# Kernel tuning notes

Measured on AMD Instinct MI355X. Metric: run time of the kernel, lower is better.

## Reference

```python
import jax, jax.numpy as jnp
import numpy as np

T, B, C, N, H = 10, 128, 512, 16, 16
D = C // H          # head dim = 32
HID = 2048          # mlp hidden = 4*dim
TAU, THR, SCALE, ALPHA_MIX = 2.0, 1.0, 0.25, 0.5
SG_ALPHA = 4.0      # surrogate sigmoid alpha

@jax.custom_vjp
def spike_fn(x):
    # heaviside forward, sigmoid surrogate backward (MyGrad / sigmoid.apply)
    return (x > 0).astype(x.dtype)

def _spike_fwd(x):
    return spike_fn(x), x

def _spike_bwd(x, g):
    s = jax.nn.sigmoid(SG_ALPHA * x)
    return (g * SG_ALPHA * s * (1.0 - s),)

spike_fn.defvjp(_spike_fwd, _spike_bwd)

def lif(x):
    # multi-step LIF over leading T axis; mem_detach=True => no BPTT through mem
    def step(mem, inp):
        mem = jax.lax.stop_gradient(mem)
        mem = mem + (inp - mem) / TAU
        s = spike_fn(mem - THR)
        mem = mem * (1.0 - jax.lax.stop_gradient(s))
        return mem, s
    return jax.lax.scan(step, jnp.zeros_like(x[0]), x)[1]

def lif_step(mem, inp):
    # single-step LIF (step=1, layer_by_layer=False); state persists across calls
    mem = jax.lax.stop_gradient(mem)
    mem = mem + (inp - mem) / TAU
    s = spike_fn(mem - THR)
    mem = mem * (1.0 - jax.lax.stop_gradient(s))
    return s, mem

def bn(x, p):
    # eval-mode BatchNorm1d over channel dim; x: (T,B,C,N), p: (4,C)=gamma,beta,mean,var
    g, b, m, v = p
    inv = g * jax.lax.rsqrt(v + 1e-5)
    return (x - m[None, None, :, None]) * inv[None, None, :, None] + b[None, None, :, None]

def conv1x1(x, W):
    # Conv1d k=1 == channel GEMM; x: (T,B,Cin,N), W: (Cout,Cin)
    return jnp.einsum('oc,tbcn->tbon', W, x)

def ssa(x, Wq, bn_q, Wk, bn_k, Wv, bn_v, Wproj, bn_proj, ti_w, ti_b):
    def qkv(W, p):
        y = lif(bn(conv1x1(x, W), p))                       # (T,B,C,N) spikes
        # faithful to torch: raw reshape (T,B,C,N)->(T,B,N,H,D) then permute
        return y.reshape(T, B, N, H, D).transpose(0, 1, 3, 2, 4)  # (T,B,H,N,D)
    q = qkv(Wq, bn_q)
    k = qkv(Wk, bn_k)
    v = qkv(Wv, bn_v)

    out0 = (q[0] @ jnp.swapaxes(k[0], -2, -1) * SCALE) @ v[0]   # (B,H,N,D)

    def step(carry, qkv_t):
        q_ti, mem1, mem2 = carry
        qt, kt, vt = qkv_t
        c = q_ti.reshape(B * H, N, D)
        c = jax.lax.conv_general_dilated(
            c, ti_w, (1,), ((2, 2),), dimension_numbers=('NCH', 'OIH', 'NCH'))
        c = c + ti_b[None, :, None]
        c = c.reshape(B, H, N, D)
        s1, mem1 = lif_step(mem1, c)
        mix = s1 * ALPHA_MIX + qt * (1.0 - ALPHA_MIX)
        s2, mem2 = lif_step(mem2, mix)
        attn = (s2 @ jnp.swapaxes(kt, -2, -1) * SCALE) @ vt
        return (s2, mem1, mem2), attn

    init = (q[0], jnp.zeros_like(q[0]), jnp.zeros_like(q[0]))
    _, outs = jax.lax.scan(step, init, (q[1:], k[1:], v[1:]))
    out = jnp.concatenate([out0[None], outs], axis=0)           # (T,B,H,N,D)

    y = jnp.swapaxes(out, 3, 4).reshape(T, B, C, N)
    y = lif(y)                                                  # attn_lif
    y = lif(bn(conv1x1(y, Wproj), bn_proj))                     # proj
    return y

def mlp(x, W1, b1, bn1, W2, b2, bn2):
    h = lif(bn(conv1x1(x, W1) + b1[None, None, :, None], bn1))
    return lif(bn(conv1x1(h, W2) + b2[None, None, :, None], bn2))

def block(x, Wq, Wk, Wv, Wproj, bn_q, bn_k, bn_v, bn_proj, ti_w, ti_b,
          W1, b1, bn1, W2, b2, bn2):
    x = x + ssa(x, Wq, bn_q, Wk, bn_k, Wv, bn_v, Wproj, bn_proj, ti_w, ti_b)
    x = x + mlp(x, W1, b1, bn1, W2, b2, bn2)
    return x

def setup_inputs() -> dict:
    key = jax.random.key(0)
    ks = jax.random.split(key, 16)

    def w(k, o, i):
        return (jax.random.normal(k, (o, i), jnp.float32) / np.float32(np.sqrt(i)))

    def bnp(k, c):
        k1, k2, k3, k4 = jax.random.split(k, 4)
        return jnp.stack([
            jax.random.uniform(k1, (c,), jnp.float32) + 0.5,   # gamma
            jax.random.normal(k2, (c,), jnp.float32) * 0.1,    # beta
            jax.random.normal(k3, (c,), jnp.float32) * 0.1,    # running mean
            jax.random.uniform(k4, (c,), jnp.float32) + 0.5,   # running var
        ])

    return {
        'x': jax.random.normal(ks[0], (T, B, C, N), jnp.float32),
        'Wq': w(ks[1], C, C), 'Wk': w(ks[2], C, C), 'Wv': w(ks[3], C, C),
        'Wproj': w(ks[4], C, C),
        'bn_q': bnp(ks[5], C), 'bn_k': bnp(ks[6], C), 'bn_v': bnp(ks[7], C),
        'bn_proj': bnp(ks[8], C),
        'ti_w': jax.random.normal(ks[9], (16, 16, 5), jnp.float32) / np.float32(np.sqrt(16 * 5)),
        'ti_b': jax.random.normal(ks[10], (16,), jnp.float32) * 0.1,
        'W1': w(ks[11], HID, C), 'b1': jax.random.normal(ks[12], (HID,), jnp.float32) * 0.1,
        'bn1': bnp(ks[13], HID),
        'W2': w(ks[14], C, HID), 'b2': jax.random.normal(ks[15], (C,), jnp.float32) * 0.1,
        'bn2': bnp(jax.random.fold_in(key, 99), C),
    }

def reference(x, Wq, Wk, Wv, Wproj, bn_q, bn_k, bn_v, bn_proj, ti_w, ti_b,
              W1, b1, bn1, W2, b2, bn2):
    return block(x, Wq, Wk, Wv, Wproj, bn_q, bn_k, bn_v, bn_proj, ti_w, ti_b,
                 W1, b1, bn1, W2, b2, bn2)
```

## Files before the change

kernel.cpp:

```cpp
#include <hip/hip_runtime.h>
#include <cstdint>
#include <cstddef>

#define T_   10
#define B_   128
#define CH_  512
#define N_   16
#define H_   16
#define HID_ 2048
#define TB_  (T_ * B_)

#define EP_QKV  0
#define EP_SPK  1
#define EP_HS   2
#define EP_OUT  3

typedef __attribute__((ext_vector_type(8))) short bf16x8;
typedef __attribute__((ext_vector_type(4))) float f32x4;
typedef unsigned short u16;
typedef unsigned long long u64;

__device__ __forceinline__ short f2b(float f) {
    uint32_t u = __float_as_uint(f);
    return (short)((u + 0x7FFFu + ((u >> 16) & 1u)) >> 16);
}
__device__ __forceinline__ float b2f(short s) {
    return __uint_as_float(((uint32_t)(uint16_t)s) << 16);
}

__global__ void fold2(const float* __restrict__ W, const float* __restrict__ bnp,
                      const float* __restrict__ eb, int M, int K, int o0,
                      short* __restrict__ Ah, short* __restrict__ Al,
                      float* __restrict__ bias) {
    int idx = blockIdx.x * 256 + threadIdx.x;
    if (idx >= M * K) return;
    int o = idx / K, k = idx - o * K;
    float g  = bnp[o];
    float be = bnp[M + o];
    float mu = bnp[2 * M + o];
    float va = bnp[3 * M + o];
    float inv = g * (1.0f / sqrtf(va + 1e-5f));
    float w = W[idx] * inv;
    short h = f2b(w);
    Ah[(size_t)(o0 + o) * K + k] = h;
    Al[(size_t)(o0 + o) * K + k] = f2b(w - b2f(h));
    if (k == 0) bias[o0 + o] = ((eb ? eb[o] : 0.0f) - mu) * inv + be;
}

__global__ __launch_bounds__(256) void splitx(
    const float* __restrict__ X, const u16* __restrict__ S,
    short* __restrict__ Bh, short* __restrict__ Bl) {
    __shared__ float xs[8192];
    const int slab = blockIdx.x;
    const int tid  = threadIdx.x;
    const int t    = slab / B_;
    const int b    = slab - t * B_;
    const float* xp = X + (size_t)slab * 8192;
    for (int i = tid; i < 2048; i += 256) {
        float4 v = *(const float4*)&xp[i * 4];
        if (S) {
            union { u16 s[4]; uint2 v; } sw;
            sw.v = *(const uint2*)&S[(size_t)b * 8192 + i * 4];
            v.x += (float)((sw.s[0] >> t) & 1);
            v.y += (float)((sw.s[1] >> t) & 1);
            v.z += (float)((sw.s[2] >> t) & 1);
            v.w += (float)((sw.s[3] >> t) & 1);
        }
        *(float4*)&xs[i * 4] = v;
    }
    __syncthreads();
    const int n = tid & 15, kc = tid >> 4;
    size_t orow = ((size_t)slab * 16 + n) * 512 + kc * 32;
#pragma unroll
    for (int i8 = 0; i8 < 4; ++i8) {
        union { short s[8]; uint4 v; } hb, lb;
#pragma unroll
        for (int j = 0; j < 8; ++j) {
            float v = xs[(kc * 32 + i8 * 8 + j) * 16 + n];
            short h = f2b(v);
            hb.s[j] = h;
            lb.s[j] = f2b(v - b2f(h));
        }
        *(uint4*)&Bh[orow + i8 * 8] = hb.v;
        *(uint4*)&Bl[orow + i8 * 8] = lb.v;
    }
}

template <int R, int GX, int EPI>
__global__ __launch_bounds__(256, 2) void gemm_bf16t(
    const short* __restrict__ Ah, const short* __restrict__ Al,
    const float* __restrict__ bias,
    const short* __restrict__ Bh, const short* __restrict__ Bl,
    u16* __restrict__ O0, u16* __restrict__ O1, u16* __restrict__ O2) {
    constexpr int KT = 512;
    __shared__ __align__(16) short BsH[6400];
    __shared__ __align__(16) short BsL[6400];
    const int tid  = threadIdx.x;
    const int lane = tid & 63;
    const int wv   = tid >> 6;
    const int fid  = blockIdx.x;
    const int xcd  = fid & 7;
    const int slot = fid >> 3;
    const int brow = slot / GX;
    const int xb   = slot - brow * GX;
    const int b    = (brow << 3) | xcd;
    const int l15  = lane & 15;
    const int q    = lane >> 4;
    const int row0 = xb * (R * 64) + wv * (R * 16);

    const int i0 = tid, i1 = tid + 256, i2 = tid + 512;
    auto gaddr = [&](int idx, int k0) -> size_t {
        int qu = idx & 3, n = (idx >> 2) & 15, t = idx >> 6;
        return ((size_t)(t * B_ + b) * 16 + n) * KT + k0 + qu * 8;
    };
    auto laddr = [&](int idx) -> int {
        int qu = idx & 3, n = (idx >> 2) & 15, t = idx >> 6;
        return (t * 16 + n) * 40 + qu * 8;
    };

    f32x4 acc[R][10];
#pragma unroll
    for (int r = 0; r < R; ++r)
#pragma unroll
        for (int t = 0; t < 10; ++t) acc[r][t] = 0.0f;

    uint4 ph0, ph1, ph2, pl0, pl1, pl2;
    ph0 = *(const uint4*)&Bh[gaddr(i0, 0)];
    pl0 = *(const uint4*)&Bl[gaddr(i0, 0)];
    ph1 = *(const uint4*)&Bh[gaddr(i1, 0)];
    pl1 = *(const uint4*)&Bl[gaddr(i1, 0)];
    if (tid < 128) {
        ph2 = *(const uint4*)&Bh[gaddr(i2, 0)];
        pl2 = *(const uint4*)&Bl[gaddr(i2, 0)];
    }

    for (int k0 = 0; k0 < KT; k0 += 32) {
        __syncthreads();
        *(uint4*)&BsH[laddr(i0)] = ph0;
        *(uint4*)&BsL[laddr(i0)] = pl0;
        *(uint4*)&BsH[laddr(i1)] = ph1;
        *(uint4*)&BsL[laddr(i1)] = pl1;
        if (tid < 128) {
            *(uint4*)&BsH[laddr(i2)] = ph2;
            *(uint4*)&BsL[laddr(i2)] = pl2;
        }
        __syncthreads();
        if (k0 + 32 < KT) {
            ph0 = *(const uint4*)&Bh[gaddr(i0, k0 + 32)];
            pl0 = *(const uint4*)&Bl[gaddr(i0, k0 + 32)];
            ph1 = *(const uint4*)&Bh[gaddr(i1, k0 + 32)];
            pl1 = *(const uint4*)&Bl[gaddr(i1, k0 + 32)];
            if (tid < 128) {
                ph2 = *(const uint4*)&Bh[gaddr(i2, k0 + 32)];
                pl2 = *(const uint4*)&Bl[gaddr(i2, k0 + 32)];
            }
        }
        bf16x8 ah[R], al[R];
#pragma unroll
        for (int r = 0; r < R; ++r) {
            size_t ga = (size_t)(row0 + r * 16 + l15) * KT + k0 + q * 8;
            ah[r] = *(const bf16x8*)&Ah[ga];
            al[r] = *(const bf16x8*)&Al[ga];
        }
#pragma unroll
        for (int t = 0; t < 10; ++t) {
            bf16x8 bh = *(const bf16x8*)&BsH[(t * 16 + l15) * 40 + q * 8];
            bf16x8 bl = *(const bf16x8*)&BsL[(t * 16 + l15) * 40 + q * 8];
#pragma unroll
            for (int r = 0; r < R; ++r) {
                acc[r][t] = __builtin_amdgcn_mfma_f32_16x16x32_bf16(ah[r], bh, acc[r][t], 0, 0, 0);
                acc[r][t] = __builtin_amdgcn_mfma_f32_16x16x32_bf16(al[r], bh, acc[r][t], 0, 0, 0);
                acc[r][t] = __builtin_amdgcn_mfma_f32_16x16x32_bf16(ah[r], bl, acc[r][t], 0, 0, 0);
            }
        }
    }

    const int tok = l15;
#pragma unroll
    for (int r = 0; r < R; ++r) {
        u16 m4[4];
#pragma unroll
        for (int reg = 0; reg < 4; ++reg) {
            const int row = row0 + r * 16 + q * 4 + reg;
            const float bsv = bias[row];
            float mem = 0.0f;
            u16 msk = 0;
#pragma unroll
            for (int t = 0; t < 10; ++t) {
                float u = acc[r][t][reg] + bsv;
                mem += (u - mem) * 0.5f;
                bool s = mem > 1.0f;
                if (s) mem = 0.0f;
                msk |= (u16)((s ? 1u : 0u) << t);
            }
            if constexpr (EPI == EP_QKV) {
                int tsr = row >> 9;
                int c   = row & 511;
                int hh  = (c & 31) >> 1;
                int dd  = ((c & 1) << 4) | tok;
                int nn  = c >> 5;
                u16* qp = (tsr == 0) ? O0 : ((tsr == 1) ? O1 : O2);
                qp[(size_t)b * 8192 + (size_t)hh * 512 + dd * 16 + nn] = msk;
            } else {
                m4[reg] = msk;
            }
        }
        if constexpr (EPI == EP_HS) {
            union { u16 s[4]; uint2 v; } pk;
            pk.s[0] = m4[0]; pk.s[1] = m4[1]; pk.s[2] = m4[2]; pk.s[3] = m4[3];
            *(uint2*)&O0[((size_t)b * 16 + tok) * 2048 + row0 + r * 16 + q * 4] = pk.v;
        }
    }
}

template <int R, int GX, int EPI, int KT>
__global__ __launch_bounds__(256, 2) void gemm_pkt(
    const short* __restrict__ Ah, const short* __restrict__ Al,
    const float* __restrict__ bias, const u16* __restrict__ Bu,
    u16* __restrict__ O0, float* __restrict__ Oout,
    const float* __restrict__ Xr, const u16* __restrict__ Sr) {
    constexpr int K8 = KT / 8;
    __shared__ __align__(16) u16 Bp[K8 * 136];
    const int tid  = threadIdx.x;
    const int lane = tid & 63;
    const int wv   = tid >> 6;
    const int fid  = blockIdx.x;
    const int xcd  = fid & 7;
    const int slot = fid >> 3;
    const int brow = slot / GX;
    const int xb   = slot - brow * GX;
    const int b    = (brow << 3) | xcd;
    const int l15  = lane & 15;
    const int q    = lane >> 4;
    const int row0 = xb * (R * 64) + wv * (R * 16);

    for (int idx = tid; idx < 16 * K8; idx += 256) {
        int kc = idx & (K8 - 1), n = idx / K8;
        *(uint4*)&Bp[kc * 136 + n * 8] =
            *(const uint4*)&Bu[((size_t)b * 16 + n) * KT + kc * 8];
    }
    __syncthreads();

    f32x4 acc[R][10];
#pragma unroll
    for (int r = 0; r < R; ++r)
#pragma unroll
        for (int t = 0; t < 10; ++t) acc[r][t] = 0.0f;

    for (int k0 = 0; k0 < KT; k0 += 32) {
        bf16x8 ah[R], al[R];
#pragma unroll
        for (int r = 0; r < R; ++r) {
            size_t ga = (size_t)(row0 + r * 16 + l15) * KT + k0 + q * 8;
            ah[r] = *(const bf16x8*)&Ah[ga];
            al[r] = *(const bf16x8*)&Al[ga];
        }
        union { uint32_t u[4]; uint4 v; } w;
        w.v = *(const uint4*)&Bp[(k0 / 8 + q) * 136 + l15 * 8];
#pragma unroll
        for (int t = 0; t < 10; ++t) {
            union { uint32_t u[4]; bf16x8 h; } bh;
#pragma unroll
            for (int j = 0; j < 4; ++j)
                bh.u[j] = ((w.u[j] >> t) & 0x00010001u) * 0x3F80u;
#pragma unroll
            for (int r = 0; r < R; ++r) {
                acc[r][t] = __builtin_amdgcn_mfma_f32_16x16x32_bf16(ah[r], bh.h, acc[r][t], 0, 0, 0);
                acc[r][t] = __builtin_amdgcn_mfma_f32_16x16x32_bf16(al[r], bh.h, acc[r][t], 0, 0, 0);
            }
        }
    }

    const int tok = l15;
#pragma unroll
    for (int r = 0; r < R; ++r) {
#pragma unroll
        for (int reg = 0; reg < 4; ++reg) {
            const int row = row0 + r * 16 + q * 4 + reg;
            const float bsv = bias[row];
            u16 sv = 0;
            if constexpr (EPI == EP_OUT) sv = Sr[(size_t)b * 8192 + (size_t)row * 16 + tok];
            float mem = 0.0f;
            u16 msk = 0;
#pragma unroll
            for (int t = 0; t < 10; ++t) {
                float u = acc[r][t][reg] + bsv;
                mem += (u - mem) * 0.5f;
                bool s = mem > 1.0f;
                if (s) mem = 0.0f;
                msk |= (u16)((s ? 1u : 0u) << t);
                if constexpr (EPI == EP_OUT) {
                    size_t off = (size_t)(t * B_ + b) * 8192 + (size_t)row * 16 + tok;
                    Oout[off] = Xr[off] + (float)((sv >> t) & 1) + (s ? 1.0f : 0.0f);
                }
            }
            if constexpr (EPI == EP_SPK) {
                O0[(size_t)b * 8192 + (size_t)row * 16 + tok] = msk;
            }
        }
    }
}

__global__ __launch_bounds__(256, 1) void scan_kernel(
    const u16* __restrict__ qs, const u16* __restrict__ ks,
    const u16* __restrict__ vs, const float* __restrict__ tiw,
    const float* __restrict__ tib, u16* __restrict__ y1pk) {
    __shared__ float qS[4][36 * 20];
    __shared__ float kS[4][32 * 20];
    __shared__ float vS[4][32 * 20];
    __shared__ float qbS[4][32 * 20];
    __shared__ float A[4][16 * 17];
    const int l  = threadIdx.x & 63;
    const int w  = threadIdx.x >> 6;
    const int b  = blockIdx.y;
    const int h  = blockIdx.x * 4 + w;
    const int n  = l & 15, dg = l >> 4;
    float* qSw  = qS[w];
    float* kSw  = kS[w];
    float* vSw  = vS[w];
    float* qbSw = qbS[w];
    float* Aw   = A[w];

    float wreg[80];
#pragma unroll
    for (int j = 0; j < 80; ++j) wreg[j] = tiw[n * 80 + j];
    const float tibr = tib[n];

    if (l < 40) { qSw[l] = 0.0f; qSw[680 + l] = 0.0f; }

    const size_t base = (size_t)b * 8192 + (size_t)h * 512 + (size_t)l * 8;
    union { u16 s[8]; uint4 v; } qw, kw, vw;
    qw.v = *(const uint4*)&qs[base];
    kw.v = *(const uint4*)&ks[base];
    vw.v = *(const uint4*)&vs[base];

#pragma unroll
    for (int j = 0; j < 8; ++j) {
        int f = l * 8 + j, d = f >> 4, m = f & 15;
        qSw[(d + 2) * 20 + m] = (float)(qw.s[j] & 1);
        kSw[d * 20 + m]       = (float)(kw.s[j] & 1);
        vSw[d * 20 + m]       = (float)(vw.s[j] & 1);
    }

    float mem1[8] = {}, mem2[8] = {}, mem3[8] = {};
    u16 ym[8] = {};

    auto attn_step = [&](int t) {
        float dots[4] = {0.0f, 0.0f, 0.0f, 0.0f};
#pragma unroll
        for (int d = 0; d < 32; ++d) {
            float qv = qSw[(d + 2) * 20 + n];
#pragma unroll
            for (int jj = 0; jj < 4; ++jj)
                dots[jj] = fmaf(qv, kSw[d * 20 + dg * 4 + jj], dots[jj]);
        }
#pragma unroll
        for (int jj = 0; jj < 4; ++jj) Aw[n * 17 + dg * 4 + jj] = dots[jj] * 0.25f;
        float o[8] = {};
#pragma unroll
        for (int m = 0; m < 16; ++m) {
            float av = Aw[n * 17 + m];
#pragma unroll
            for (int dd = 0; dd < 8; ++dd)
                o[dd] = fmaf(av, vSw[(dg * 8 + dd) * 20 + m], o[dd]);
        }
#pragma unroll
        for (int dd = 0; dd < 8; ++dd) {
            mem3[dd] += (o[dd] - mem3[dd]) * 0.5f;
            bool s3 = mem3[dd] > 1.0f;
            if (s3) mem3[dd] = 0.0f;
            ym[dd] |= (u16)((s3 ? 1u : 0u) << t);
        }
    };

    attn_step(0);

    for (int t = 1; t < T_; ++t) {
#pragma unroll
        for (int j = 0; j < 8; ++j) {
            int f = l * 8 + j, d = f >> 4, m = f & 15;
            qbSw[d * 20 + m] = (float)((qw.s[j] >> t) & 1);
            kSw[d * 20 + m]  = (float)((kw.s[j] >> t) & 1);
            vSw[d * 20 + m]  = (float)((vw.s[j] >> t) & 1);
        }
        float c[8];
#pragma unroll
        for (int dd = 0; dd < 8; ++dd) c[dd] = tibr;
#pragma unroll
        for (int x = 0; x < 12; ++x) {
            const float* rp = &qSw[(dg * 8 + x) * 20];
            float qrow[16];
            *(float4*)&qrow[0]  = *(const float4*)&rp[0];
            *(float4*)&qrow[4]  = *(const float4*)&rp[4];
            *(float4*)&qrow[8]  = *(const float4*)&rp[8];
            *(float4*)&qrow[12] = *(const float4*)&rp[12];
#pragma unroll
            for (int k = 0; k < 5; ++k) {
                const int o = x - k;
                if (o >= 0 && o < 8) {
#pragma unroll
                    for (int i = 0; i < 16; ++i)
                        c[o] = fmaf(wreg[i * 5 + k], qrow[i], c[o]);
                }
            }
        }
#pragma unroll
        for (int dd = 0; dd < 8; ++dd) {
            mem1[dd] += (c[dd] - mem1[dd]) * 0.5f;
            bool s1 = mem1[dd] > 1.0f;
            if (s1) mem1[dd] = 0.0f;
            float qb = qbSw[(dg * 8 + dd) * 20 + n];
            float mix = 0.5f * (s1 ? 1.0f : 0.0f) + 0.5f * qb;
            mem2[dd] += (mix - mem2[dd]) * 0.5f;
            bool s2 = mem2[dd] > 1.0f;
            if (s2) mem2[dd] = 0.0f;
            qSw[(dg * 8 + dd + 2) * 20 + n] = s2 ? 1.0f : 0.0f;
        }
        attn_step(t);
    }

    union { u16 s[8]; uint4 v; } yv;
#pragma unroll
    for (int dd = 0; dd < 8; ++dd) yv.s[dd] = ym[dd];
    *(uint4*)&y1pk[((size_t)b * 16 + n) * 512 + h * 32 + dg * 8] = yv.v;
}

extern "C" void kernel_launch(void* const* d_in, const int* in_sizes, int n_in,
                              void* d_out, int out_size, void* d_ws, size_t ws_size,
                              hipStream_t stream) {
    const float* x    = (const float*)d_in[0];
    const float* Wq   = (const float*)d_in[1];
    const float* Wk   = (const float*)d_in[2];
    const float* Wv   = (const float*)d_in[3];
    const float* Wp   = (const float*)d_in[4];
    const float* bnq  = (const float*)d_in[5];
    const float* bnk  = (const float*)d_in[6];
    const float* bnv  = (const float*)d_in[7];
    const float* bnpj = (const float*)d_in[8];
    const float* tiw  = (const float*)d_in[9];
    const float* tib  = (const float*)d_in[10];
    const float* W1   = (const float*)d_in[11];
    const float* b1   = (const float*)d_in[12];
    const float* bn1  = (const float*)d_in[13];
    const float* W2   = (const float*)d_in[14];
    const float* b2   = (const float*)d_in[15];
    const float* bn2  = (const float*)d_in[16];
    float* out = (float*)d_out;

    char* ws = (char*)d_ws;
    size_t cur = 0;
    auto alloc = [&](size_t bytes) -> void* {
        void* p = ws + cur;
        cur = (cur + bytes + 255) & ~(size_t)255;
        return p;
    };
    const size_t PKQ = (size_t)B_ * 8192;
    u16* qpk  = (u16*)alloc(4 * PKQ * 2);
    u16* kpk  = qpk + PKQ;
    u16* vpk  = qpk + 2 * PKQ;
    u16* y1pk = qpk + 3 * PKQ;
    u16* hspk = qpk;
    u16* spk  = (u16*)alloc(PKQ * 2);
    short* BhT = (short*)alloc((size_t)TB_ * 16 * 512 * 2);
    short* BlT = (short*)alloc((size_t)TB_ * 16 * 512 * 2);
    short* Ah_qkv = (short*)alloc((size_t)1536 * 512 * 2);
    short* Al_qkv = (short*)alloc((size_t)1536 * 512 * 2);
    short* Ah_p   = (short*)alloc((size_t)512 * 512 * 2);
    short* Al_p   = (short*)alloc((size_t)512 * 512 * 2);
    short* Ah_1   = (short*)alloc((size_t)2048 * 512 * 2);
    short* Al_1   = (short*)alloc((size_t)2048 * 512 * 2);
    short* Ah_2   = (short*)alloc((size_t)512 * 2048 * 2);
    short* Al_2   = (short*)alloc((size_t)512 * 2048 * 2);
    float* bs_qkv = (float*)alloc(1536 * 4);
    float* bs_p   = (float*)alloc(512 * 4);
    float* bs_1   = (float*)alloc(2048 * 4);
    float* bs_2   = (float*)alloc(512 * 4);

    fold2<<<1024, 256, 0, stream>>>(Wq, bnq, nullptr, 512, 512, 0,    Ah_qkv, Al_qkv, bs_qkv);
    fold2<<<1024, 256, 0, stream>>>(Wk, bnk, nullptr, 512, 512, 512,  Ah_qkv, Al_qkv, bs_qkv);
    fold2<<<1024, 256, 0, stream>>>(Wv, bnv, nullptr, 512, 512, 1024, Ah_qkv, Al_qkv, bs_qkv);
    fold2<<<1024, 256, 0, stream>>>(Wp, bnpj, nullptr, 512, 512, 0,   Ah_p, Al_p, bs_p);
    fold2<<<4096, 256, 0, stream>>>(W1, bn1, b1, 2048, 512, 0,        Ah_1, Al_1, bs_1);
    fold2<<<4096, 256, 0, stream>>>(W2, bn2, b2, 512, 2048, 0,        Ah_2, Al_2, bs_2);

    splitx<<<TB_, 256, 0, stream>>>(x, nullptr, BhT, BlT);
    gemm_bf16t<2, 12, EP_QKV><<<12 * B_, 256, 0, stream>>>(
        Ah_qkv, Al_qkv, bs_qkv, BhT, BlT, qpk, kpk, vpk);
    scan_kernel<<<dim3(4, B_), 256, 0, stream>>>(qpk, kpk, vpk, tiw, tib, y1pk);
    gemm_pkt<2, 4, EP_SPK, 512><<<4 * B_, 256, 0, stream>>>(
        Ah_p, Al_p, bs_p, y1pk, spk, nullptr, nullptr, nullptr);

    splitx<<<TB_, 256, 0, stream>>>(x, spk, BhT, BlT);
    gemm_bf16t<2, 16, EP_HS><<<16 * B_, 256, 0, stream>>>(
        Ah_1, Al_1, bs_1, BhT, BlT, hspk, nullptr, nullptr);
    gemm_pkt<2, 4, EP_OUT, 2048><<<4 * B_, 256, 0, stream>>>(
        Ah_2, Al_2, bs_2, hspk, nullptr, out, x, spk);
}
```

Measured before the change: 570.2 us.

## Double-buffer B tile in LDS and prefetch A fragments one step ahead

The GEMM's shared-memory B tile becomes double-buffered, which drops one of the two barriers per K-step. The A-operand register fragments for the next K-step are now loaded one iteration early, so global load latency overlaps with the MFMA work. This doubles LDS use to about 51 KB per block, which may limit occupancy under launch_bounds(256,2), and it raises register pressure from the extra A fragment copies.

```diff
diff --git a/kernel.cpp b/kernel.cpp
--- a/kernel.cpp
+++ b/kernel.cpp
@@ -93,8 +93,8 @@
     const short* __restrict__ Bh, const short* __restrict__ Bl,
     u16* __restrict__ O0, u16* __restrict__ O1, u16* __restrict__ O2) {
     constexpr int KT = 512;
-    __shared__ __align__(16) short BsH[6400];
-    __shared__ __align__(16) short BsL[6400];
+    __shared__ __align__(16) short BsH[2][6400];
+    __shared__ __align__(16) short BsL[2][6400];
     const int tid  = threadIdx.x;
     const int lane = tid & 63;
     const int wv   = tid >> 6;
@@ -133,16 +133,23 @@
         ph2 = *(const uint4*)&Bh[gaddr(i2, 0)];
         pl2 = *(const uint4*)&Bl[gaddr(i2, 0)];
     }
-
+    bf16x8 ahc[R], alc[R], ahn[R], aln[R];
+#pragma unroll
+    for (int r = 0; r < R; ++r) {
+        size_t ga = (size_t)(row0 + r * 16 + l15) * KT + q * 8;
+        ahc[r] = *(const bf16x8*)&Ah[ga];
+        alc[r] = *(const bf16x8*)&Al[ga];
+    }
+
+    int cur = 0;
     for (int k0 = 0; k0 < KT; k0 += 32) {
-        __syncthreads();
-        *(uint4*)&BsH[laddr(i0)] = ph0;
-        *(uint4*)&BsL[laddr(i0)] = pl0;
-        *(uint4*)&BsH[laddr(i1)] = ph1;
-        *(uint4*)&BsL[laddr(i1)] = pl1;
+        *(uint4*)&BsH[cur][laddr(i0)] = ph0;
+        *(uint4*)&BsL[cur][laddr(i0)] = pl0;
+        *(uint4*)&BsH[cur][laddr(i1)] = ph1;
+        *(uint4*)&BsL[cur][laddr(i1)] = pl1;
         if (tid < 128) {
-            *(uint4*)&BsH[laddr(i2)] = ph2;
-            *(uint4*)&BsL[laddr(i2)] = pl2;
+            *(uint4*)&BsH[cur][laddr(i2)] = ph2;
+            *(uint4*)&BsL[cur][laddr(i2)] = pl2;
         }
         __syncthreads();
         if (k0 + 32 < KT) {
@@ -154,25 +161,27 @@
                 ph2 = *(const uint4*)&Bh[gaddr(i2, k0 + 32)];
                 pl2 = *(const uint4*)&Bl[gaddr(i2, k0 + 32)];
             }
-        }
-        bf16x8 ah[R], al[R];
-#pragma unroll
-        for (int r = 0; r < R; ++r) {
-            size_t ga = (size_t)(row0 + r * 16 + l15) * KT + k0 + q * 8;
-            ah[r] = *(const bf16x8*)&Ah[ga];
-            al[r] = *(const bf16x8*)&Al[ga];
+#pragma unroll
+            for (int r = 0; r < R; ++r) {
+                size_t ga = (size_t)(row0 + r * 16 + l15) * KT + (k0 + 32) + q * 8;
+                ahn[r] = *(const bf16x8*)&Ah[ga];
+                aln[r] = *(const bf16x8*)&Al[ga];
+            }
         }
 #pragma unroll
         for (int t = 0; t < 10; ++t) {
-            bf16x8 bh = *(const bf16x8*)&BsH[(t * 16 + l15) * 40 + q * 8];
-            bf16x8 bl = *(const bf16x8*)&BsL[(t * 16 + l15) * 40 + q * 8];
+            bf16x8 bh = *(const bf16x8*)&BsH[cur][(t * 16 + l15) * 40 + q * 8];
+            bf16x8 bl = *(const bf16x8*)&BsL[cur][(t * 16 + l15) * 40 + q * 8];
 #pragma unroll
             for (int r = 0; r < R; ++r) {
-                acc[r][t] = __builtin_amdgcn_mfma_f32_16x16x32_bf16(ah[r], bh, acc[r][t], 0, 0, 0);
-                acc[r][t] = __builtin_amdgcn_mfma_f32_16x16x32_bf16(al[r], bh, acc[r][t], 0, 0, 0);
-                acc[r][t] = __builtin_amdgcn_mfma_f32_16x16x32_bf16(ah[r], bl, acc[r][t], 0, 0, 0);
-            }
-        }
+                acc[r][t] = __builtin_amdgcn_mfma_f32_16x16x32_bf16(ahc[r], bh, acc[r][t], 0, 0, 0);
+                acc[r][t] = __builtin_amdgcn_mfma_f32_16x16x32_bf16(alc[r], bh, acc[r][t], 0, 0, 0);
+                acc[r][t] = __builtin_amdgcn_mfma_f32_16x16x32_bf16(ahc[r], bl, acc[r][t], 0, 0, 0);
+            }
+        }
+#pragma unroll
+        for (int r = 0; r < R; ++r) { ahc[r] = ahn[r]; alc[r] = aln[r]; }
+        cur ^= 1;
     }
 
     const int tok = l15;
```

Measured after the change: 563.1 us. No clear change (-1.2%).
